# Optimization experiments

Hardware: AMD Instinct MI355X
Metric: run time of the kernel (lower is better)

## Reference

```python
import jax, jax.numpy as jnp
import numpy as np

D_MODEL = 1024
NUM_HEADS = 16
D_K = D_MODEL // NUM_HEADS
BATCH = 8
SEQ = 1024


def setup_inputs() -> dict:
    key = jax.random.key(0)
    ks = jax.random.split(key, 16)
    s = 1.0 / np.sqrt(D_MODEL)
    def lin(i):
        W = jax.random.uniform(ks[i], (D_MODEL, D_MODEL), jnp.float32, -s, s)
        b = jax.random.uniform(ks[i + 1], (D_MODEL,), jnp.float32, -s, s)
        return W, b
    Wq, bq = lin(0)
    Wk, bk = lin(2)
    Wv, bv = lin(4)
    Wg, bg = lin(6)
    Wbeta, bbeta = lin(8)
    Wo, bo = lin(10)
    X = jax.random.normal(ks[12], (BATCH, SEQ, D_MODEL), jnp.float32)
    Y = jax.random.normal(ks[13], (BATCH, SEQ, D_MODEL), jnp.float32)
    return dict(X=X, Y=Y, Wq=Wq, bq=bq, Wk=Wk, bk=bk, Wv=Wv, bv=bv,
                Wg=Wg, bg=bg, Wbeta=Wbeta, bbeta=bbeta, Wo=Wo, bo=bo)


def _split_heads(x):
    b, s, _ = x.shape
    return x.reshape(b, s, NUM_HEADS, D_K).transpose(0, 2, 1, 3)  # [b,h,s,d_k]


def _attend(q_in, kv_in, Wq, bq, Wk, bk, Wv, bv, Wg, bg, Wbeta, bbeta, Wo, bo):
    Q = _split_heads(q_in @ Wq + bq)
    K = _split_heads(kv_in @ Wk + bk)
    V = _split_heads(kv_in @ Wv + bv)
    scores = jnp.einsum('bhqd,bhkd->bhqk', Q, K) / jnp.sqrt(jnp.float32(D_K))
    attn = jax.nn.softmax(scores, axis=-1)
    ctx = jnp.einsum('bhqk,bhkd->bhqd', attn, V)
    b, h, s, d = ctx.shape
    ctx = ctx.transpose(0, 2, 1, 3).reshape(b, s, h * d)
    out = (ctx @ Wg + bg) * jnp.sqrt(jnp.float32(D_K)) + (ctx @ Wbeta + bbeta)
    return out @ Wo + bo


def reference(X, Y, Wq, bq, Wk, bk, Wv, bv, Wg, bg, Wbeta, bbeta, Wo, bo):
    params = (Wq, bq, Wk, bk, Wv, bv, Wg, bg, Wbeta, bbeta, Wo, bo)
    Y_new = _attend(X, Y, *params)   # pass 1: queries from X, keys/values from Y
    X_new = _attend(Y_new, X, *params)  # pass 2: queries from new Y, kv from original X
    return (X_new, Y_new)
```

## Files before the change

kernel.cpp:

```cpp
#include <hip/hip_runtime.h>

typedef unsigned short u16;
typedef __bf16 bf16x8 __attribute__((ext_vector_type(8)));
typedef float f32x4 __attribute__((ext_vector_type(4)));
typedef float f32x16 __attribute__((ext_vector_type(16)));
typedef u16 u16x4 __attribute__((ext_vector_type(4)));
typedef unsigned int u32x4v __attribute__((ext_vector_type(4)));

#define LOG2E_OVER_8 0.18033688011112043f

__device__ __forceinline__ u16 f2bf(float f) {
  union { float f; unsigned int u; } x{f};
  unsigned int r = (x.u + 0x7fffu + ((x.u >> 16) & 1u)) >> 16;
  return (u16)r;
}

__device__ __forceinline__ float bf2f(u16 v) {
  union { unsigned int u; float f; } x;
  x.u = ((unsigned int)v) << 16;
  return x.f;
}

__device__ __forceinline__ unsigned cvtpk(float a, float b) {
  unsigned r;
  asm("v_cvt_pk_bf16_f32 %0, %1, %2" : "=v"(r) : "v"(a), "v"(b));
  return r;
}

__device__ __forceinline__ void gld16(const void* g, void* l) {
  __builtin_amdgcn_global_load_lds((const __attribute__((address_space(1))) unsigned int*)g,
                                   (__attribute__((address_space(3))) unsigned int*)l,
                                   16, 0, 0);
}

__global__ void prep_w(const float* __restrict__ Wq, const float* __restrict__ Wk,
                       const float* __restrict__ Wv, const float* __restrict__ Wg,
                       const float* __restrict__ Wb, const float* __restrict__ Wo,
                       u16* __restrict__ Wqt, u16* __restrict__ Wkt, u16* __restrict__ Wvt,
                       u16* __restrict__ Wcn, u16* __restrict__ Wot)
{
  __shared__ float tile[32][33];
  const int m = blockIdx.z;
  const int nb = blockIdx.x * 32, kb = blockIdx.y * 32;
  const int tx = threadIdx.x, ty = threadIdx.y;
  const float* src = (m == 0) ? Wq : (m == 1) ? Wk : (m == 2) ? Wv : (m == 3) ? Wg : Wo;
  u16* dst = (m == 0) ? Wqt : (m == 1) ? Wkt : (m == 2) ? Wvt : (m == 3) ? Wcn : Wot;
#pragma unroll
  for (int i = 0; i < 4; ++i) {
    const int k = kb + ty + i * 8;
    float v = src[k * 1024 + nb + tx];
    if (m == 3) v = 8.0f * v + Wb[k * 1024 + nb + tx];
    if (m == 0) v *= LOG2E_OVER_8;
    if (m == 3) dst[k * 1024 + nb + tx] = f2bf(v);
    else        tile[ty + i * 8][tx] = v;
  }
  __syncthreads();
  if (m != 3) {
#pragma unroll
    for (int i = 0; i < 4; ++i) {
      const int r = ty + i * 8;
      dst[(nb + r) * 1024 + kb + tx] = f2bf(tile[tx][r]);
    }
  }
}

__global__ void prep_b(const float* __restrict__ bq, const float* __restrict__ bg,
                       const float* __restrict__ bb,
                       float* __restrict__ bqs, float* __restrict__ bcs)
{
  const int i = blockIdx.x * 256 + threadIdx.x;
  if (i < 1024) {
    bqs[i] = bq[i] * LOG2E_OVER_8;
    bcs[i] = 8.0f * bg[i] + bb[i];
  }
}

__global__ void cvt2_bf16(const float* __restrict__ in0, u16* __restrict__ out0,
                          const float* __restrict__ in1, u16* __restrict__ out1, int n)
{
  int i = (blockIdx.x * blockDim.x + threadIdx.x) * 4;
  const int stride = gridDim.x * blockDim.x * 4;
  for (; i < n; i += stride) {
    const float4 v0 = *reinterpret_cast<const float4*>(in0 + i);
    u16x4 o0;
    o0.x = f2bf(v0.x); o0.y = f2bf(v0.y); o0.z = f2bf(v0.z); o0.w = f2bf(v0.w);
    *reinterpret_cast<u16x4*>(out0 + i) = o0;
    const float4 v1 = *reinterpret_cast<const float4*>(in1 + i);
    u16x4 o1;
    o1.x = f2bf(v1.x); o1.y = f2bf(v1.y); o1.z = f2bf(v1.z); o1.w = f2bf(v1.w);
    *reinterpret_cast<u16x4*>(out1 + i) = o1;
  }
}

template<int EPI, int NB>
__device__ __forceinline__ void gemm_body(int bid0, u16* lA, u16* lB,
                                          const u16* __restrict__ A,
                                          const u16* __restrict__ Bt,
                                          const float* __restrict__ bias,
                                          u16* __restrict__ outb, float* __restrict__ outf)
{
  int bid = (bid0 & 7) * NB + (bid0 >> 3);
  const int row0 = (bid >> 3) * 128;
  const int col0 = (bid & 7) * 128;
  const int t = threadIdx.x;
  const int w = t >> 6, lane = t & 63;
  const int l15 = lane & 15, l4 = lane >> 4;
  const int wr = w >> 1, wc = w & 1;
  const int l7 = l15 & 7;

  const u16* gA[4];
  const u16* gB[4];
#pragma unroll
  for (int k2 = 0; k2 < 4; ++k2) {
    const int c = k2 * 256 + t;
    const int r = c >> 3;
    const int sc = ((c & 7) ^ (r & 7)) * 8;
    gA[k2] = A + (row0 + r) * 1024 + sc;
    gB[k2] = Bt + (col0 + r) * 1024 + sc;
  }

  f32x4 acc[4][4] = {};

  for (int kt = 0; kt < 1024; kt += 64) {
#pragma unroll
    for (int k2 = 0; k2 < 4; ++k2) {
      gld16(gA[k2] + kt, lA + (k2 * 256 + w * 64) * 8);
      gld16(gB[k2] + kt, lB + (k2 * 256 + w * 64) * 8);
    }
    __syncthreads();
    bf16x8 aF[4][2], bF[4][2];
#pragma unroll
    for (int m = 0; m < 4; ++m)
#pragma unroll
      for (int ks = 0; ks < 2; ++ks)
        aF[m][ks] = *reinterpret_cast<const bf16x8*>(
            &lA[(wr * 64 + m * 16 + l15) * 64 + ((ks * 4 + l4) ^ l7) * 8]);
#pragma unroll
    for (int n = 0; n < 4; ++n)
#pragma unroll
      for (int ks = 0; ks < 2; ++ks)
        bF[n][ks] = *reinterpret_cast<const bf16x8*>(
            &lB[(wc * 64 + n * 16 + l15) * 64 + ((ks * 4 + l4) ^ l7) * 8]);
#pragma unroll
    for (int m = 0; m < 4; ++m)
#pragma unroll
      for (int n = 0; n < 4; ++n) {
        acc[m][n] = __builtin_amdgcn_mfma_f32_16x16x32_bf16(aF[m][0], bF[n][0], acc[m][n], 0, 0, 0);
        acc[m][n] = __builtin_amdgcn_mfma_f32_16x16x32_bf16(aF[m][1], bF[n][1], acc[m][n], 0, 0, 0);
      }
    __syncthreads();
  }

  float bv[4];
#pragma unroll
  for (int n = 0; n < 4; ++n)
    bv[n] = (EPI == 4) ? 0.0f : bias[col0 + wc * 64 + n * 16 + l15];
#pragma unroll
  for (int m = 0; m < 4; ++m) {
#pragma unroll
    for (int n = 0; n < 4; ++n) {
      const int c = col0 + wc * 64 + n * 16 + l15;
#pragma unroll
      for (int j = 0; j < 4; ++j) {
        const int r = row0 + wr * 64 + m * 16 + l4 * 4 + j;
        const float v = acc[m][n][j] + bv[n];
        if constexpr (EPI == 0 || EPI == 4) {
          outb[r * 1024 + c] = f2bf(v);
        } else if constexpr (EPI == 1) {
          outf[r * 1024 + c] = v;
          outb[r * 1024 + c] = f2bf(v);
        } else if constexpr (EPI == 2) {
          const int bi = r >> 10, s = r & 1023;
          const int h = c >> 6, d = c & 63;
          outb[((bi * 16 + h) * 64 + d) * 1024 + s] = f2bf(v);
        } else {
          outf[r * 1024 + c] = v;
        }
      }
    }
  }
}

__device__ __forceinline__ void bias_body(int bb, const float* __restrict__ bcs,
                                          const u16* __restrict__ Wot,
                                          const float* __restrict__ bo,
                                          float* __restrict__ bco)
{
  const int t = threadIdx.x, w = t >> 6, l = t & 63;
  const int n = bb * 4 + w;
  const u16* row = Wot + n * 1024;
  float a = 0.f;
#pragma unroll
  for (int i = 0; i < 16; ++i) a += bcs[l + 64 * i] * bf2f(row[l + 64 * i]);
#pragma unroll
  for (int d = 1; d < 64; d <<= 1) a += __shfl_xor(a, d);
  if (l == 0) bco[n] = a + bo[n];
}

template<int EPI, int NB = 64>
__global__ __launch_bounds__(256, 2)
void gemm_k(const u16* __restrict__ A, const u16* __restrict__ Bt,
            const float* __restrict__ bias,
            u16* __restrict__ outb, float* __restrict__ outf)
{
  __shared__ u16 lA[128 * 64];
  __shared__ u16 lB[128 * 64];
  gemm_body<EPI, NB>((int)blockIdx.x, lA, lB, A, Bt, bias, outb, outf);
}

__global__ __launch_bounds__(256, 2)
void gemm5_k(const u16* __restrict__ Xb, const u16* __restrict__ Yb,
             const u16* __restrict__ Wqt, const float* __restrict__ bqs,
             const u16* __restrict__ Wkt, const float* __restrict__ bk,
             const u16* __restrict__ Wvt, const float* __restrict__ bv,
             u16* __restrict__ Qb, u16* __restrict__ Kb, u16* __restrict__ Vt,
             u16* __restrict__ Kb2, u16* __restrict__ Vt2,
             const u16* __restrict__ Wot, const u16* __restrict__ Wcn,
             u16* __restrict__ Wcot,
             const float* __restrict__ bcs, const float* __restrict__ bo,
             float* __restrict__ bco)
{
  __shared__ u16 lA[128 * 64];
  __shared__ u16 lB[128 * 64];
  const int id = (int)blockIdx.x;
  if (id < 512)       gemm_body<0, 64>(id,        lA, lB, Xb, Wqt, bqs, Qb, nullptr);
  else if (id < 1024) gemm_body<0, 64>(id - 512,  lA, lB, Yb, Wkt, bk, Kb, nullptr);
  else if (id < 1536) gemm_body<2, 64>(id - 1024, lA, lB, Yb, Wvt, bv, Vt, nullptr);
  else if (id < 2048) gemm_body<0, 64>(id - 1536, lA, lB, Xb, Wkt, bk, Kb2, nullptr);
  else if (id < 2560) gemm_body<2, 64>(id - 2048, lA, lB, Xb, Wvt, bv, Vt2, nullptr);
  else if (id < 2624) gemm_body<4, 8>(id - 2560,  lA, lB, Wot, Wcn, nullptr, Wcot, nullptr);
  else                bias_body(id - 2624, bcs, Wot, bo, bco);
}

__global__ __launch_bounds__(256, 2)
void gemm3_k(const u16* __restrict__ A0, const u16* __restrict__ B0,
             const float* __restrict__ c0, u16* __restrict__ o0,
             const u16* __restrict__ A1, const u16* __restrict__ B1,
             const float* __restrict__ c1, u16* __restrict__ o1,
             const u16* __restrict__ A2, const u16* __restrict__ B2,
             const float* __restrict__ c2, u16* __restrict__ o2)
{
  __shared__ u16 lA[128 * 64];
  __shared__ u16 lB[128 * 64];
  const int id = (int)blockIdx.x;
  if (id < 512)       gemm_body<0, 64>(id,        lA, lB, A0, B0, c0, o0, nullptr);
  else if (id < 1024) gemm_body<0, 64>(id - 512,  lA, lB, A1, B1, c1, o1, nullptr);
  else                gemm_body<2, 64>(id - 1024, lA, lB, A2, B2, c2, o2, nullptr);
}

__global__ __launch_bounds__(256, 4)
void attn_k(const u16* __restrict__ Q, const u16* __restrict__ K,
            const u16* __restrict__ Vt, u16* __restrict__ ctx)
{
  __shared__ u16 lK[64 * 72];
  __shared__ u16 lV[64 * 72];
  __shared__ float lsumI[4][32];
  const int id = (int)blockIdx.x;
  const int xcd = id & 7, o = id >> 3;
  const int pair = xcd * 16 + (o >> 3);
  const int qt = o & 7;
  const int b = pair >> 4, h = pair & 15;
  const int t = threadIdx.x, w = t >> 6, lane = t & 63;
  const int l31 = lane & 31, hi = lane >> 5;
  const int q0 = qt * 128 + w * 32;
  const u16* Qp = Q + (size_t)b * (1024 * 1024) + h * 64;
  const u16* Kp = K + (size_t)b * (1024 * 1024) + h * 64;
  const u16* Vp = Vt + (size_t)(b * 16 + h) * (64 * 1024);

  const int r0 = t >> 3, c0 = (t & 7) * 8;

  bf16x8 bQ[4];
#pragma unroll
  for (int ks = 0; ks < 4; ++ks)
    bQ[ks] = *reinterpret_cast<const bf16x8*>(&Qp[(q0 + l31) * 1024 + ks * 16 + hi * 8]);

  f32x16 acc[2] = {};
  float lsum = 0.f;

  bf16x8 sK0, sK1, sV0, sV1;
  sK0 = *reinterpret_cast<const bf16x8*>(&Kp[(r0) * 1024 + c0]);
  sK1 = *reinterpret_cast<const bf16x8*>(&Kp[(r0 + 32) * 1024 + c0]);
  sV0 = *reinterpret_cast<const bf16x8*>(&Vp[r0 * 1024 + c0]);
  sV1 = *reinterpret_cast<const bf16x8*>(&Vp[(r0 + 32) * 1024 + c0]);

  for (int it = 0; it < 16; ++it) {
    const int kv0 = it * 64;
    __syncthreads();
    *reinterpret_cast<bf16x8*>(&lK[r0 * 72 + c0]) = sK0;
    *reinterpret_cast<bf16x8*>(&lK[(r0 + 32) * 72 + c0]) = sK1;
    *reinterpret_cast<bf16x8*>(&lV[r0 * 72 + c0]) = sV0;
    *reinterpret_cast<bf16x8*>(&lV[(r0 + 32) * 72 + c0]) = sV1;
    __syncthreads();
    if (it + 1 < 16) {
      const int nk = kv0 + 64;
      sK0 = *reinterpret_cast<const bf16x8*>(&Kp[(nk + r0) * 1024 + c0]);
      sK1 = *reinterpret_cast<const bf16x8*>(&Kp[(nk + r0 + 32) * 1024 + c0]);
      sV0 = *reinterpret_cast<const bf16x8*>(&Vp[r0 * 1024 + nk + c0]);
      sV1 = *reinterpret_cast<const bf16x8*>(&Vp[(r0 + 32) * 1024 + nk + c0]);
    }

    f32x16 sS[2] = {};
    __builtin_amdgcn_s_setprio(1);
#pragma unroll
    for (int tt = 0; tt < 2; ++tt) {
#pragma unroll
      for (int ks = 0; ks < 4; ++ks) {
        const bf16x8 aK = *reinterpret_cast<const bf16x8*>(
            &lK[(tt * 32 + l31) * 72 + ks * 16 + hi * 8]);
        sS[tt] = __builtin_amdgcn_mfma_f32_32x32x16_bf16(aK, bQ[ks], sS[tt], 0, 0, 0);
      }
    }
    __builtin_amdgcn_s_setprio(0);

    unsigned pa[2][2][4];
#pragma unroll
    for (int tt = 0; tt < 2; ++tt) {
      float p[16];
      float s0 = 0.f, s1 = 0.f, s2 = 0.f, s3 = 0.f;
#pragma unroll
      for (int r = 0; r < 16; r += 4) {
        p[r]     = __builtin_amdgcn_exp2f(sS[tt][r]);
        p[r + 1] = __builtin_amdgcn_exp2f(sS[tt][r + 1]);
        p[r + 2] = __builtin_amdgcn_exp2f(sS[tt][r + 2]);
        p[r + 3] = __builtin_amdgcn_exp2f(sS[tt][r + 3]);
        s0 += p[r]; s1 += p[r + 1]; s2 += p[r + 2]; s3 += p[r + 3];
      }
      lsum += (s0 + s1) + (s2 + s3);
      unsigned wv[8];
#pragma unroll
      for (int i = 0; i < 8; ++i) wv[i] = cvtpk(p[2 * i], p[2 * i + 1]);
#pragma unroll
      for (int c = 0; c < 2; ++c) {
        unsigned a0 = wv[4 * c + 0], b0 = wv[4 * c + 2];
        unsigned a1 = wv[4 * c + 1], b1 = wv[4 * c + 3];
        asm("v_permlane32_swap_b32 %0, %1" : "+v"(a0), "+v"(b0));
        asm("v_permlane32_swap_b32 %0, %1" : "+v"(a1), "+v"(b1));
        pa[tt][c][0] = a0;
        pa[tt][c][1] = a1;
        pa[tt][c][2] = b0;
        pa[tt][c][3] = b1;
      }
    }

    __builtin_amdgcn_s_setprio(1);
#pragma unroll
    for (int tt = 0; tt < 2; ++tt)
#pragma unroll
      for (int c = 0; c < 2; ++c) {
        u32x4v pw;
        pw.x = pa[tt][c][0]; pw.y = pa[tt][c][1];
        pw.z = pa[tt][c][2]; pw.w = pa[tt][c][3];
        const bf16x8 aP = __builtin_bit_cast(bf16x8, pw);
#pragma unroll
        for (int dt = 0; dt < 2; ++dt) {
          const bf16x8 bV = *reinterpret_cast<const bf16x8*>(
              &lV[(dt * 32 + l31) * 72 + tt * 32 + c * 16 + hi * 8]);
          acc[dt] = __builtin_amdgcn_mfma_f32_32x32x16_bf16(aP, bV, acc[dt], 0, 0, 0);
        }
      }
    __builtin_amdgcn_s_setprio(0);
  }

  const float ltot = lsum + __shfl_xor(lsum, 32);
  if (hi == 0) lsumI[w][l31] = 1.0f / ltot;
  u16* Cp = ctx + (size_t)b * (1024 * 1024) + h * 64;
#pragma unroll
  for (int dt = 0; dt < 2; ++dt)
#pragma unroll
    for (int r = 0; r < 16; ++r) {
      const int q = (r & 3) + 8 * (r >> 2) + 4 * hi;
      const float inv = lsumI[w][q];
      Cp[(q0 + q) * 1024 + dt * 32 + l31] = f2bf(acc[dt][r] * inv);
    }
}

extern "C" void kernel_launch(void* const* d_in, const int* in_sizes, int n_in,
                              void* d_out, int out_size, void* d_ws, size_t ws_size,
                              hipStream_t stream)
{
  (void)in_sizes; (void)n_in; (void)out_size;
  const float* X  = (const float*)d_in[0];
  const float* Y  = (const float*)d_in[1];
  const float* Wq = (const float*)d_in[2];
  const float* bq = (const float*)d_in[3];
  const float* Wk = (const float*)d_in[4];
  const float* bk = (const float*)d_in[5];
  const float* Wv = (const float*)d_in[6];
  const float* bv = (const float*)d_in[7];
  const float* Wg = (const float*)d_in[8];
  const float* bg = (const float*)d_in[9];
  const float* Wb = (const float*)d_in[10];
  const float* bb = (const float*)d_in[11];
  const float* Wo = (const float*)d_in[12];
  const float* bo = (const float*)d_in[13];
  float* out = (float*)d_out;
  char* ws = (char*)d_ws;
  const size_t MB = 1024ull * 1024ull;

  u16* Wqt = (u16*)(ws + 0 * MB);
  u16* Wkt = (u16*)(ws + 2 * MB);
  u16* Wvt = (u16*)(ws + 4 * MB);
  u16* Wcn = (u16*)(ws + 6 * MB);
  u16* Wot = (u16*)(ws + 8 * MB);
  u16* Wcot = (u16*)(ws + 10 * MB);
  u16* Xb = (u16*)(ws + 12 * MB);
  u16* Yb = (u16*)(ws + 28 * MB);
  u16* Qb = (u16*)(ws + 44 * MB);
  u16* Kb = (u16*)(ws + 60 * MB);
  u16* Vt = (u16*)(ws + 76 * MB);
  u16* Cx = (u16*)(ws + 92 * MB);
  float* bqs = (float*)(ws + 108 * MB);
  float* bcs = (float*)(ws + 108 * MB + 4096);
  float* bco = (float*)(ws + 108 * MB + 8192);
  u16* Kb2 = (u16*)(ws + 110 * MB);
  u16* Vt2 = (u16*)(ws + 126 * MB);
  const int NEL = 8 * 1024 * 1024;
  const bool hoist = ws_size >= 143 * MB;

  prep_w<<<dim3(32, 32, 5), dim3(32, 8), 0, stream>>>(Wq, Wk, Wv, Wg, Wb, Wo,
                                                      Wqt, Wkt, Wvt, Wcn, Wot);
  prep_b<<<4, 256, 0, stream>>>(bq, bg, bb, bqs, bcs);
  cvt2_bf16<<<2048, 256, 0, stream>>>(X, Xb, Y, Yb, NEL);

  if (hoist) {
    gemm5_k<<<2880, 256, 0, stream>>>(Xb, Yb, Wqt, bqs, Wkt, bk, Wvt, bv,
                                      Qb, Kb, Vt, Kb2, Vt2,
                                      Wot, Wcn, Wcot, bcs, bo, bco);
    attn_k<<<1024, 256, 0, stream>>>(Qb, Kb, Vt, Cx);
    gemm_k<1><<<512, 256, 0, stream>>>(Cx, Wcot, bco, Yb, out + NEL);
    gemm_k<0><<<512, 256, 0, stream>>>(Yb, Wqt, bqs, Qb, nullptr);
    attn_k<<<1024, 256, 0, stream>>>(Qb, Kb2, Vt2, Cx);
  } else {
    gemm5_k<<<2624, 256, 0, stream>>>(Xb, Yb, Wqt, bqs, Wkt, bk, Wvt, bv,
                                      Qb, Kb, Vt, Kb, Vt,
                                      Wot, Wcn, Wcot, bcs, bo, bco);
    attn_k<<<1024, 256, 0, stream>>>(Qb, Kb, Vt, Cx);
    gemm_k<1><<<512, 256, 0, stream>>>(Cx, Wcot, bco, Yb, out + NEL);
    gemm3_k<<<1536, 256, 0, stream>>>(Yb, Wqt, bqs, Qb,
                                      Xb, Wkt, bk, Kb,
                                      Xb, Wvt, bv, Vt);
    attn_k<<<1024, 256, 0, stream>>>(Qb, Kb, Vt, Cx);
  }
  gemm_k<3><<<512, 256, 0, stream>>>(Cx, Wcot, bco, nullptr, out);
}
```

Baseline: 287.4 us.

## Widen attention KV tile to 128 and drop hoisted pass-2 K/V projection

The attention kernel now stages 128 keys and values per loop iteration, processed as two 64-wide halves. This halves the number of barrier pairs and global prefetch rounds per block, at the cost of more shared memory and registers, which may reduce occupancy at 4 blocks per CU. The host path no longer picks a hoisted variant by workspace size. It always computes the pass-2 K/V projection after pass 1 in a combined three-GEMM launch, which removes the extra K/V buffers but also gives up overlapping that work with the pass-1 projections.

```diff
diff --git a/kernel.cpp b/kernel.cpp
--- a/kernel.cpp
+++ b/kernel.cpp
@@ -209,16 +209,15 @@
 }
 
 __global__ __launch_bounds__(256, 2)
-void gemm5_k(const u16* __restrict__ Xb, const u16* __restrict__ Yb,
-             const u16* __restrict__ Wqt, const float* __restrict__ bqs,
-             const u16* __restrict__ Wkt, const float* __restrict__ bk,
-             const u16* __restrict__ Wvt, const float* __restrict__ bv,
-             u16* __restrict__ Qb, u16* __restrict__ Kb, u16* __restrict__ Vt,
-             u16* __restrict__ Kb2, u16* __restrict__ Vt2,
-             const u16* __restrict__ Wot, const u16* __restrict__ Wcn,
-             u16* __restrict__ Wcot,
-             const float* __restrict__ bcs, const float* __restrict__ bo,
-             float* __restrict__ bco)
+void gemmp1_k(const u16* __restrict__ Xb, const u16* __restrict__ Yb,
+              const u16* __restrict__ Wqt, const float* __restrict__ bqs,
+              const u16* __restrict__ Wkt, const float* __restrict__ bk,
+              const u16* __restrict__ Wvt, const float* __restrict__ bv,
+              u16* __restrict__ Qb, u16* __restrict__ Kb, u16* __restrict__ Vt,
+              const u16* __restrict__ Wot, const u16* __restrict__ Wcn,
+              u16* __restrict__ Wcot,
+              const float* __restrict__ bcs, const float* __restrict__ bo,
+              float* __restrict__ bco)
 {
   __shared__ u16 lA[128 * 64];
   __shared__ u16 lB[128 * 64];
@@ -226,19 +225,17 @@
   if (id < 512)       gemm_body<0, 64>(id,        lA, lB, Xb, Wqt, bqs, Qb, nullptr);
   else if (id < 1024) gemm_body<0, 64>(id - 512,  lA, lB, Yb, Wkt, bk, Kb, nullptr);
   else if (id < 1536) gemm_body<2, 64>(id - 1024, lA, lB, Yb, Wvt, bv, Vt, nullptr);
-  else if (id < 2048) gemm_body<0, 64>(id - 1536, lA, lB, Xb, Wkt, bk, Kb2, nullptr);
-  else if (id < 2560) gemm_body<2, 64>(id - 2048, lA, lB, Xb, Wvt, bv, Vt2, nullptr);
-  else if (id < 2624) gemm_body<4, 8>(id - 2560,  lA, lB, Wot, Wcn, nullptr, Wcot, nullptr);
-  else                bias_body(id - 2624, bcs, Wot, bo, bco);
+  else if (id < 1600) gemm_body<4, 8>(id - 1536,  lA, lB, Wot, Wcn, nullptr, Wcot, nullptr);
+  else                bias_body(id - 1600, bcs, Wot, bo, bco);
 }
 
 __global__ __launch_bounds__(256, 2)
-void gemm3_k(const u16* __restrict__ A0, const u16* __restrict__ B0,
-             const float* __restrict__ c0, u16* __restrict__ o0,
-             const u16* __restrict__ A1, const u16* __restrict__ B1,
-             const float* __restrict__ c1, u16* __restrict__ o1,
-             const u16* __restrict__ A2, const u16* __restrict__ B2,
-             const float* __restrict__ c2, u16* __restrict__ o2)
+void gemmp2_k(const u16* __restrict__ A0, const u16* __restrict__ B0,
+              const float* __restrict__ c0, u16* __restrict__ o0,
+              const u16* __restrict__ A1, const u16* __restrict__ B1,
+              const float* __restrict__ c1, u16* __restrict__ o1,
+              const u16* __restrict__ A2, const u16* __restrict__ B2,
+              const float* __restrict__ c2, u16* __restrict__ o2)
 {
   __shared__ u16 lA[128 * 64];
   __shared__ u16 lB[128 * 64];
@@ -252,8 +249,8 @@
 void attn_k(const u16* __restrict__ Q, const u16* __restrict__ K,
             const u16* __restrict__ Vt, u16* __restrict__ ctx)
 {
-  __shared__ u16 lK[64 * 72];
-  __shared__ u16 lV[64 * 72];
+  __shared__ u16 lK[128 * 72];
+  __shared__ u16 lV[2][64 * 72];
   __shared__ float lsumI[4][32];
   const int id = (int)blockIdx.x;
   const int xcd = id & 7, o = id >> 3;
@@ -277,88 +274,105 @@
   f32x16 acc[2] = {};
   float lsum = 0.f;
 
-  bf16x8 sK0, sK1, sV0, sV1;
-  sK0 = *reinterpret_cast<const bf16x8*>(&Kp[(r0) * 1024 + c0]);
-  sK1 = *reinterpret_cast<const bf16x8*>(&Kp[(r0 + 32) * 1024 + c0]);
-  sV0 = *reinterpret_cast<const bf16x8*>(&Vp[r0 * 1024 + c0]);
-  sV1 = *reinterpret_cast<const bf16x8*>(&Vp[(r0 + 32) * 1024 + c0]);
-
-  for (int it = 0; it < 16; ++it) {
-    const int kv0 = it * 64;
+  bf16x8 sK[4], sV[4];
+#pragma unroll
+  for (int i = 0; i < 4; ++i)
+    sK[i] = *reinterpret_cast<const bf16x8*>(&Kp[(r0 + 32 * i) * 1024 + c0]);
+#pragma unroll
+  for (int j = 0; j < 2; ++j)
+#pragma unroll
+    for (int i = 0; i < 2; ++i)
+      sV[j * 2 + i] = *reinterpret_cast<const bf16x8*>(
+          &Vp[(r0 + 32 * i) * 1024 + j * 64 + c0]);
+
+  for (int it = 0; it < 8; ++it) {
+    const int kv0 = it * 128;
     __syncthreads();
-    *reinterpret_cast<bf16x8*>(&lK[r0 * 72 + c0]) = sK0;
-    *reinterpret_cast<bf16x8*>(&lK[(r0 + 32) * 72 + c0]) = sK1;
-    *reinterpret_cast<bf16x8*>(&lV[r0 * 72 + c0]) = sV0;
-    *reinterpret_cast<bf16x8*>(&lV[(r0 + 32) * 72 + c0]) = sV1;
+#pragma unroll
+    for (int i = 0; i < 4; ++i)
+      *reinterpret_cast<bf16x8*>(&lK[(r0 + 32 * i) * 72 + c0]) = sK[i];
+#pragma unroll
+    for (int j = 0; j < 2; ++j)
+#pragma unroll
+      for (int i = 0; i < 2; ++i)
+        *reinterpret_cast<bf16x8*>(&lV[j][(r0 + 32 * i) * 72 + c0]) = sV[j * 2 + i];
     __syncthreads();
-    if (it + 1 < 16) {
-      const int nk = kv0 + 64;
-      sK0 = *reinterpret_cast<const bf16x8*>(&Kp[(nk + r0) * 1024 + c0]);
-      sK1 = *reinterpret_cast<const bf16x8*>(&Kp[(nk + r0 + 32) * 1024 + c0]);
-      sV0 = *reinterpret_cast<const bf16x8*>(&Vp[r0 * 1024 + nk + c0]);
-      sV1 = *reinterpret_cast<const bf16x8*>(&Vp[(r0 + 32) * 1024 + nk + c0]);
-    }
-
-    f32x16 sS[2] = {};
-    __builtin_amdgcn_s_setprio(1);
-#pragma unroll
-    for (int tt = 0; tt < 2; ++tt) {
-#pragma unroll
-      for (int ks = 0; ks < 4; ++ks) {
-        const bf16x8 aK = *reinterpret_cast<const bf16x8*>(
-            &lK[(tt * 32 + l31) * 72 + ks * 16 + hi * 8]);
-        sS[tt] = __builtin_amdgcn_mfma_f32_32x32x16_bf16(aK, bQ[ks], sS[tt], 0, 0, 0);
-      }
-    }
-    __builtin_amdgcn_s_setprio(0);
-
-    unsigned pa[2][2][4];
-#pragma unroll
-    for (int tt = 0; tt < 2; ++tt) {
-      float p[16];
-      float s0 = 0.f, s1 = 0.f, s2 = 0.f, s3 = 0.f;
-#pragma unroll
-      for (int r = 0; r < 16; r += 4) {
-        p[r]     = __builtin_amdgcn_exp2f(sS[tt][r]);
-        p[r + 1] = __builtin_amdgcn_exp2f(sS[tt][r + 1]);
-        p[r + 2] = __builtin_amdgcn_exp2f(sS[tt][r + 2]);
-        p[r + 3] = __builtin_amdgcn_exp2f(sS[tt][r + 3]);
-        s0 += p[r]; s1 += p[r + 1]; s2 += p[r + 2]; s3 += p[r + 3];
-      }
-      lsum += (s0 + s1) + (s2 + s3);
-      unsigned wv[8];
-#pragma unroll
-      for (int i = 0; i < 8; ++i) wv[i] = cvtpk(p[2 * i], p[2 * i + 1]);
-#pragma unroll
-      for (int c = 0; c < 2; ++c) {
-        unsigned a0 = wv[4 * c + 0], b0 = wv[4 * c + 2];
-        unsigned a1 = wv[4 * c + 1], b1 = wv[4 * c + 3];
-        asm("v_permlane32_swap_b32 %0, %1" : "+v"(a0), "+v"(b0));
-        asm("v_permlane32_swap_b32 %0, %1" : "+v"(a1), "+v"(b1));
-        pa[tt][c][0] = a0;
-        pa[tt][c][1] = a1;
-        pa[tt][c][2] = b0;
-        pa[tt][c][3] = b1;
-      }
-    }
-
-    __builtin_amdgcn_s_setprio(1);
-#pragma unroll
-    for (int tt = 0; tt < 2; ++tt)
-#pragma unroll
-      for (int c = 0; c < 2; ++c) {
-        u32x4v pw;
-        pw.x = pa[tt][c][0]; pw.y = pa[tt][c][1];
-        pw.z = pa[tt][c][2]; pw.w = pa[tt][c][3];
-        const bf16x8 aP = __builtin_bit_cast(bf16x8, pw);
-#pragma unroll
-        for (int dt = 0; dt < 2; ++dt) {
-          const bf16x8 bV = *reinterpret_cast<const bf16x8*>(
-              &lV[(dt * 32 + l31) * 72 + tt * 32 + c * 16 + hi * 8]);
-          acc[dt] = __builtin_amdgcn_mfma_f32_32x32x16_bf16(aP, bV, acc[dt], 0, 0, 0);
+    if (it + 1 < 8) {
+      const int nk = kv0 + 128;
+#pragma unroll
+      for (int i = 0; i < 4; ++i)
+        sK[i] = *reinterpret_cast<const bf16x8*>(&Kp[(nk + r0 + 32 * i) * 1024 + c0]);
+#pragma unroll
+      for (int j = 0; j < 2; ++j)
+#pragma unroll
+        for (int i = 0; i < 2; ++i)
+          sV[j * 2 + i] = *reinterpret_cast<const bf16x8*>(
+              &Vp[(r0 + 32 * i) * 1024 + nk + j * 64 + c0]);
+    }
+
+#pragma unroll
+    for (int half = 0; half < 2; ++half) {
+      f32x16 sS[2] = {};
+      __builtin_amdgcn_s_setprio(1);
+#pragma unroll
+      for (int tt = 0; tt < 2; ++tt) {
+#pragma unroll
+        for (int ks = 0; ks < 4; ++ks) {
+          const bf16x8 aK = *reinterpret_cast<const bf16x8*>(
+              &lK[(half * 64 + tt * 32 + l31) * 72 + ks * 16 + hi * 8]);
+          sS[tt] = __builtin_amdgcn_mfma_f32_32x32x16_bf16(aK, bQ[ks], sS[tt], 0, 0, 0);
         }
       }
-    __builtin_amdgcn_s_setprio(0);
+      __builtin_amdgcn_s_setprio(0);
+
+      unsigned pa[2][2][4];
+#pragma unroll
+      for (int tt = 0; tt < 2; ++tt) {
+        float p[16];
+        float s0 = 0.f, s1 = 0.f, s2 = 0.f, s3 = 0.f;
+#pragma unroll
+        for (int r = 0; r < 16; r += 4) {
+          p[r]     = __builtin_amdgcn_exp2f(sS[tt][r]);
+          p[r + 1] = __builtin_amdgcn_exp2f(sS[tt][r + 1]);
+          p[r + 2] = __builtin_amdgcn_exp2f(sS[tt][r + 2]);
+          p[r + 3] = __builtin_amdgcn_exp2f(sS[tt][r + 3]);
+          s0 += p[r]; s1 += p[r + 1]; s2 += p[r + 2]; s3 += p[r + 3];
+        }
+        lsum += (s0 + s1) + (s2 + s3);
+        unsigned wv[8];
+#pragma unroll
+        for (int i = 0; i < 8; ++i) wv[i] = cvtpk(p[2 * i], p[2 * i + 1]);
+#pragma unroll
+        for (int c = 0; c < 2; ++c) {
+          unsigned a0 = wv[4 * c + 0], b0 = wv[4 * c + 2];
+          unsigned a1 = wv[4 * c + 1], b1 = wv[4 * c + 3];
+          asm("v_permlane32_swap_b32 %0, %1" : "+v"(a0), "+v"(b0));
+          asm("v_permlane32_swap_b32 %0, %1" : "+v"(a1), "+v"(b1));
+          pa[tt][c][0] = a0;
+          pa[tt][c][1] = a1;
+          pa[tt][c][2] = b0;
+          pa[tt][c][3] = b1;
+        }
+      }
+
+      __builtin_amdgcn_s_setprio(1);
+#pragma unroll
+      for (int tt = 0; tt < 2; ++tt)
+#pragma unroll
+        for (int c = 0; c < 2; ++c) {
+          u32x4v pw;
+          pw.x = pa[tt][c][0]; pw.y = pa[tt][c][1];
+          pw.z = pa[tt][c][2]; pw.w = pa[tt][c][3];
+          const bf16x8 aP = __builtin_bit_cast(bf16x8, pw);
+#pragma unroll
+          for (int dt = 0; dt < 2; ++dt) {
+            const bf16x8 bV = *reinterpret_cast<const bf16x8*>(
+                &lV[half][(dt * 32 + l31) * 72 + tt * 32 + c * 16 + hi * 8]);
+            acc[dt] = __builtin_amdgcn_mfma_f32_32x32x16_bf16(aP, bV, acc[dt], 0, 0, 0);
+          }
+        }
+      __builtin_amdgcn_s_setprio(0);
+    }
   }
 
   const float ltot = lsum + __shfl_xor(lsum, 32);
@@ -378,7 +392,7 @@
                               void* d_out, int out_size, void* d_ws, size_t ws_size,
                               hipStream_t stream)
 {
-  (void)in_sizes; (void)n_in; (void)out_size;
+  (void)in_sizes; (void)n_in; (void)out_size; (void)ws_size;
   const float* X  = (const float*)d_in[0];
   const float* Y  = (const float*)d_in[1];
   const float* Wq = (const float*)d_in[2];
@@ -412,34 +426,21 @@
   float* bqs = (float*)(ws + 108 * MB);
   float* bcs = (float*)(ws + 108 * MB + 4096);
   float* bco = (float*)(ws + 108 * MB + 8192);
-  u16* Kb2 = (u16*)(ws + 110 * MB);
-  u16* Vt2 = (u16*)(ws + 126 * MB);
   const int NEL = 8 * 1024 * 1024;
-  const bool hoist = ws_size >= 143 * MB;
 
   prep_w<<<dim3(32, 32, 5), dim3(32, 8), 0, stream>>>(Wq, Wk, Wv, Wg, Wb, Wo,
                                                       Wqt, Wkt, Wvt, Wcn, Wot);
   prep_b<<<4, 256, 0, stream>>>(bq, bg, bb, bqs, bcs);
   cvt2_bf16<<<2048, 256, 0, stream>>>(X, Xb, Y, Yb, NEL);
 
-  if (hoist) {
-    gemm5_k<<<2880, 256, 0, stream>>>(Xb, Yb, Wqt, bqs, Wkt, bk, Wvt, bv,
-                                      Qb, Kb, Vt, Kb2, Vt2,
-                                      Wot, Wcn, Wcot, bcs, bo, bco);
-    attn_k<<<1024, 256, 0, stream>>>(Qb, Kb, Vt, Cx);
-    gemm_k<1><<<512, 256, 0, stream>>>(Cx, Wcot, bco, Yb, out + NEL);
-    gemm_k<0><<<512, 256, 0, stream>>>(Yb, Wqt, bqs, Qb, nullptr);
-    attn_k<<<1024, 256, 0, stream>>>(Qb, Kb2, Vt2, Cx);
-  } else {
-    gemm5_k<<<2624, 256, 0, stream>>>(Xb, Yb, Wqt, bqs, Wkt, bk, Wvt, bv,
-                                      Qb, Kb, Vt, Kb, Vt,
-                                      Wot, Wcn, Wcot, bcs, bo, bco);
-    attn_k<<<1024, 256, 0, stream>>>(Qb, Kb, Vt, Cx);
-    gemm_k<1><<<512, 256, 0, stream>>>(Cx, Wcot, bco, Yb, out + NEL);
-    gemm3_k<<<1536, 256, 0, stream>>>(Yb, Wqt, bqs, Qb,
-                                      Xb, Wkt, bk, Kb,
-                                      Xb, Wvt, bv, Vt);
-    attn_k<<<1024, 256, 0, stream>>>(Qb, Kb, Vt, Cx);
-  }
+  gemmp1_k<<<1856, 256, 0, stream>>>(Xb, Yb, Wqt, bqs, Wkt, bk, Wvt, bv,
+                                     Qb, Kb, Vt, Wot, Wcn, Wcot, bcs, bo, bco);
+  attn_k<<<1024, 256, 0, stream>>>(Qb, Kb, Vt, Cx);
+  gemm_k<1><<<512, 256, 0, stream>>>(Cx, Wcot, bco, Yb, out + NEL);
+
+  gemmp2_k<<<1536, 256, 0, stream>>>(Yb, Wqt, bqs, Qb,
+                                     Xb, Wkt, bk, Kb,
+                                     Xb, Wvt, bv, Vt);
+  attn_k<<<1024, 256, 0, stream>>>(Qb, Kb, Vt, Cx);
   gemm_k<3><<<512, 256, 0, stream>>>(Cx, Wcot, bco, nullptr, out);
 }
```

Result: slower. 356.5 us (+24.1%).
